# Kernel optimization log

Hardware: AMD Instinct MI355X
Metric: run time of the kernel (lower is better)

## Reference

```python
import jax, jax.numpy as jnp
import numpy as np

D_MODEL = 1024
N_HEADS = 16
EPS = 1e-5


def layernorm(x, w, b):
    mu = jnp.mean(x, axis=-1, keepdims=True)
    var = jnp.mean(jnp.square(x - mu), axis=-1, keepdims=True)
    return (x - mu) * jax.lax.rsqrt(var + EPS) * w + b


def setup_inputs() -> dict:
    key = jax.random.key(0)
    ks = jax.random.split(key, 8)
    n, s, d = 2, 2048, D_MODEL
    x = jax.random.normal(ks[0], (n, s, d), dtype=jnp.float32)
    padding_mask = jax.random.bernoulli(ks[1], 0.9, (n, s))
    # Linear weights stored as [in, out] (transpose of torch layout; same math)
    qkv_w = jax.random.normal(ks[2], (d, 3 * d), dtype=jnp.float32) / np.sqrt(d)
    qkv_b = jnp.zeros((3 * d,), dtype=jnp.float32)
    out_w = jax.random.normal(ks[3], (d, d), dtype=jnp.float32) / np.sqrt(d)
    out_b = jnp.zeros((d,), dtype=jnp.float32)
    ln_in_w = jnp.ones((d,), dtype=jnp.float32)
    ln_in_b = jnp.zeros((d,), dtype=jnp.float32)
    ln_out_w = jnp.ones((d,), dtype=jnp.float32)
    ln_out_b = jnp.zeros((d,), dtype=jnp.float32)
    return {"x": x, "padding_mask": padding_mask,
            "ln_in_w": ln_in_w, "ln_in_b": ln_in_b,
            "qkv_w": qkv_w, "qkv_b": qkv_b,
            "out_w": out_w, "out_b": out_b,
            "ln_out_w": ln_out_w, "ln_out_b": ln_out_b}


def reference(x, padding_mask, ln_in_w, ln_in_b, qkv_w, qkv_b, out_w, out_b, ln_out_w, ln_out_b):
    n, s, d = x.shape
    h = N_HEADS
    hd = d // h
    xn = layernorm(x, ln_in_w, ln_in_b)
    qkv = (xn @ qkv_w + qkv_b).reshape(n, s, 3, h, hd)  # [n,s,3,h,hd]
    q, k, v = qkv[:, :, 0], qkv[:, :, 1], qkv[:, :, 2]
    # [n,h,t,T]
    attn_logits = jnp.einsum('nthd,nThd->nhtT', q, k) / np.sqrt(hd).astype(np.float32)
    attn_logits = jnp.where(padding_mask[:, None, None, :], attn_logits, jnp.float32(-1e30))
    attn_weights = jax.nn.softmax(attn_logits, axis=-1)
    attn = jnp.einsum('nhtT,nThd->nthd', attn_weights, v)  # [n,t,h,hd]
    attn_vec = attn.reshape(n, s, d)
    return layernorm(attn_vec @ out_w + out_b, ln_out_w, ln_out_b)
```

## Files before the change

kernel.cpp:

```cpp
#include <hip/hip_runtime.h>
#include <math.h>

#define D_MODEL 1024
#define SEQ     2048
#define NBATCH  2
#define NTOK    (NBATCH * SEQ)
#define NH      16
#define HD      64

typedef float f32x4 __attribute__((ext_vector_type(4)));
typedef short bf16x8 __attribute__((ext_vector_type(8)));
typedef short bf16x4 __attribute__((ext_vector_type(4)));

__device__ __forceinline__ unsigned short f2bf(float f) {
  unsigned u = __builtin_bit_cast(unsigned, f);
  u += 0x7FFFu + ((u >> 16) & 1u);
  return (unsigned short)(u >> 16);
}

__device__ __forceinline__ unsigned cvt_pk_bf16(float lo, float hi) {
  unsigned d;
  asm("v_cvt_pk_bf16_f32 %0, %1, %2" : "=v"(d) : "v"(lo), "v"(hi));
  return d;
}

__device__ __forceinline__ f32x4 mfma16(bf16x4 a, bf16x4 b, f32x4 c) {
  return __builtin_amdgcn_mfma_f32_16x16x16bf16_1k(a, b, c, 0, 0, 0);
}

__device__ __forceinline__ void gload16(const void* g, void* l) {
  __builtin_amdgcn_global_load_lds(
      (const __attribute__((address_space(1))) void*)g,
      (__attribute__((address_space(3))) void*)l, 16, 0, 0);
}

__global__ void mask_detect_kernel(const unsigned char* __restrict__ m,
                                   int* __restrict__ flag) {
  __shared__ int c1s, c3s;
  if (threadIdx.x == 0) { c1s = 0; c3s = 0; }
  __syncthreads();
  int c1 = 0, c3 = 0;
  for (int i = threadIdx.x; i < NTOK; i += 256) {
    unsigned char v = m[i];
    if (v) {
      if ((i & 3) == 1) c1++;
      if ((i & 3) == 3) c3++;
    }
  }
  if (c1) atomicAdd(&c1s, c1);
  if (c3) atomicAdd(&c3s, c3);
  __syncthreads();
  if (threadIdx.x == 0) *flag = (c1s > 0) ? 1 : ((c3s > 0) ? 2 : 0);
}

__global__ void mask_convert_kernel(const void* __restrict__ m,
                                    const int* __restrict__ flag,
                                    float* __restrict__ maskMul) {
  int i = blockIdx.x * 256 + threadIdx.x;
  if (i >= NTOK) return;
  int f = *flag;
  bool on;
  if (f == 1)      on = ((const unsigned char*)m)[i] != 0;
  else if (f == 2) on = ((const float*)m)[i] != 0.0f;
  else             on = ((const int*)m)[i] != 0;
  maskMul[i] = on ? 1.0f : 0.0f;
}

__device__ inline float block_reduce_sum(float v, float* red) {
  #pragma unroll
  for (int s = 1; s < 64; s <<= 1) v += __shfl_xor(v, s);
  int wid = threadIdx.x >> 6, lane = threadIdx.x & 63;
  if (lane == 0) red[wid] = v;
  __syncthreads();
  float t = red[0] + red[1] + red[2] + red[3];
  __syncthreads();
  return t;
}

template <bool BF16OUT>
__global__ __launch_bounds__(256) void ln_kernel(const float* __restrict__ x,
                                                 const float* __restrict__ w,
                                                 const float* __restrict__ b,
                                                 void* __restrict__ yv) {
  __shared__ float red[4];
  int row = blockIdx.x;
  int tid = threadIdx.x;
  float4 v = ((const float4*)(x + (size_t)row * D_MODEL))[tid];
  float s = v.x + v.y + v.z + v.w;
  float tot = block_reduce_sum(s, red);
  float mu = tot * (1.0f / D_MODEL);
  float dx = v.x - mu, dy = v.y - mu, dz = v.z - mu, dw = v.w - mu;
  float sq = dx * dx + dy * dy + dz * dz + dw * dw;
  float tot2 = block_reduce_sum(sq, red);
  float inv = rsqrtf(tot2 * (1.0f / D_MODEL) + 1e-5f);
  float4 wv = ((const float4*)w)[tid];
  float4 bv = ((const float4*)b)[tid];
  float4 o;
  o.x = dx * inv * wv.x + bv.x;
  o.y = dy * inv * wv.y + bv.y;
  o.z = dz * inv * wv.z + bv.z;
  o.w = dw * inv * wv.w + bv.w;
  if constexpr (BF16OUT) {
    ushort4 o4 = {f2bf(o.x), f2bf(o.y), f2bf(o.z), f2bf(o.w)};
    ((ushort4*)((unsigned short*)yv + (size_t)row * D_MODEL))[tid] = o4;
  } else {
    ((float4*)((float*)yv + (size_t)row * D_MODEL))[tid] = o;
  }
}

__global__ __launch_bounds__(256) void transpose_convert_kernel(
    const float* __restrict__ W, unsigned short* __restrict__ WT, int K, int N) {
  __shared__ float t[64][65];
  int k0 = blockIdx.y * 64, n0 = blockIdx.x * 64;
  int tid = threadIdx.x;
  int rr = tid >> 4, cc = (tid & 15) * 4;
  #pragma unroll
  for (int i = 0; i < 4; i++) {
    int rk = i * 16 + rr;
    float4 v = *(const float4*)&W[(size_t)(k0 + rk) * N + n0 + cc];
    t[rk][cc + 0] = v.x; t[rk][cc + 1] = v.y; t[rk][cc + 2] = v.z; t[rk][cc + 3] = v.w;
  }
  __syncthreads();
  #pragma unroll
  for (int i = 0; i < 4; i++) {
    int rn = i * 16 + rr;
    ushort4 o = {f2bf(t[cc + 0][rn]), f2bf(t[cc + 1][rn]),
                 f2bf(t[cc + 2][rn]), f2bf(t[cc + 3][rn])};
    *(ushort4*)&WT[(size_t)(n0 + rn) * K + k0 + cc] = o;
  }
}

__global__ __launch_bounds__(256) void v_transpose_kernel(
    const unsigned short* __restrict__ qkv, unsigned short* __restrict__ Vt) {
  __shared__ unsigned short t[64][66];
  int s0 = blockIdx.x * 64;
  int h = blockIdx.y, n = blockIdx.z;
  int tid = threadIdx.x;
  #pragma unroll
  for (int i = 0; i < 2; i++) {
    int ch = i * 256 + tid;
    int sr = ch >> 3, c8 = (ch & 7) * 8;
    const unsigned short* src =
        qkv + (size_t)(n * SEQ + s0 + sr) * 3072 + 2048 + h * 64 + c8;
    uint4 v = *(const uint4*)src;
    unsigned short tmp[8];
    *(uint4*)tmp = v;
    #pragma unroll
    for (int j = 0; j < 8; j++) t[sr][c8 + j] = tmp[j];
  }
  __syncthreads();
  #pragma unroll
  for (int i = 0; i < 2; i++) {
    int ch = i * 256 + tid;
    int d = ch >> 3, s8 = (ch & 7) * 8;
    unsigned short tmp[8];
    #pragma unroll
    for (int j = 0; j < 8; j++) tmp[j] = t[s8 + j][d];
    unsigned short* dst =
        Vt + ((size_t)((n * NH + h) * HD) + d) * SEQ + s0 + s8;
    *(uint4*)dst = *(const uint4*)tmp;
  }
}

template <typename OutT>
__global__ __launch_bounds__(256) void gemm_mfma_kernel(
    const unsigned short* __restrict__ A, const unsigned short* __restrict__ BT,
    const float* __restrict__ bias, OutT* __restrict__ C, int M, int N, int K) {
  __shared__ __align__(16) char As[16384];
  __shared__ __align__(16) char Bs[16384];
  int tid = threadIdx.x;
  int lane = tid & 63, w = tid >> 6;
  int r = lane & 15, g = lane >> 4;
  int wm = w >> 1, wn = w & 1;
  int m0 = blockIdx.y * 128, n0 = blockIdx.x * 128;
  f32x4 acc[4][4] = {};

  const char* Ab = (const char*)A;
  const char* Bb = (const char*)BT;
  for (int k0 = 0; k0 < K; k0 += 64) {
    __syncthreads();
    #pragma unroll
    for (int i = 0; i < 4; i++) {
      int chb = i * 256 + w * 64;
      int ch = chb + lane;
      int row = ch >> 3, cb = (ch & 7) ^ (row & 7);
      gload16(Ab + (((size_t)(m0 + row) * K + k0) << 1) + (cb << 4), As + chb * 16);
      gload16(Bb + (((size_t)(n0 + row) * K + k0) << 1) + (cb << 4), Bs + chb * 16);
    }
    __syncthreads();
    #pragma unroll
    for (int s = 0; s < 2; s++) {
      bf16x8 af[4], bfr[4];
      #pragma unroll
      for (int mt = 0; mt < 4; mt++) {
        int arow = wm * 64 + mt * 16 + r;
        int cb = (s * 4 + g) ^ (arow & 7);
        af[mt] = *(const bf16x8*)(As + arow * 128 + cb * 16);
      }
      #pragma unroll
      for (int nt = 0; nt < 4; nt++) {
        int brow = wn * 64 + nt * 16 + r;
        int cb = (s * 4 + g) ^ (brow & 7);
        bfr[nt] = *(const bf16x8*)(Bs + brow * 128 + cb * 16);
      }
      #pragma unroll
      for (int mt = 0; mt < 4; mt++)
        #pragma unroll
        for (int nt = 0; nt < 4; nt++)
          acc[mt][nt] = __builtin_amdgcn_mfma_f32_16x16x32_bf16(
              af[mt], bfr[nt], acc[mt][nt], 0, 0, 0);
    }
  }
  #pragma unroll
  for (int nt = 0; nt < 4; nt++) {
    int col = n0 + wn * 64 + nt * 16 + r;
    float bv = bias[col];
    #pragma unroll
    for (int mt = 0; mt < 4; mt++) {
      #pragma unroll
      for (int rr = 0; rr < 4; rr++) {
        int row = m0 + wm * 64 + mt * 16 + g * 4 + rr;
        float v = acc[mt][nt][rr] + bv;
        if constexpr (sizeof(OutT) == 2) {
          C[(size_t)row * N + col] = (OutT)f2bf(v);
        } else {
          C[(size_t)row * N + col] = v;
        }
      }
    }
  }
}

__global__ __launch_bounds__(512, 4) void attn_mfma_kernel(
    const unsigned short* __restrict__ qkv, const unsigned short* __restrict__ Vt,
    const float* __restrict__ maskMulG, unsigned short* __restrict__ av) {
  __shared__ __align__(16) char Q_s[16384];
  __shared__ __align__(16) char K_s[2][8192];
  __shared__ __align__(16) char V_s[2][8192];
  int tid = threadIdx.x;
  int lane = tid & 63, w = tid >> 6;
  int r = lane & 15, g = lane >> 4;
  int qt = blockIdx.x, h = blockIdx.y, bn = blockIdx.z;
  size_t tok0 = (size_t)bn * SEQ;

  const char* qb = (const char*)qkv + (((tok0 + qt * 128) * 3072) + h * 64) * 2;
  const char* kb0 = (const char*)qkv + ((tok0 * 3072) + 1024 + h * 64) * 2;
  const char* vb0 = (const char*)Vt + (((size_t)(bn * NH + h) * HD) * SEQ) * 2;

  #pragma unroll
  for (int i = 0; i < 2; i++) {
    int chb = i * 512 + w * 64;
    int ch = chb + lane;
    int row = ch >> 3, cb = (ch & 7) ^ (row & 7);
    gload16(qb + (size_t)row * 6144 + (cb << 4), Q_s + chb * 16);
  }
  auto stage_kv = [&](int kt, int buf) {
    int chb = w * 64;
    int ch = chb + lane;
    int row = ch >> 3, cb = (ch & 7) ^ (row & 7);
    gload16(kb0 + (size_t)(kt * 64 + row) * 6144 + (cb << 4), K_s[buf] + chb * 16);
    gload16(vb0 + (size_t)row * 4096 + (size_t)kt * 128 + (cb << 4), V_s[buf] + chb * 16);
  };
  stage_kv(0, 0);
  __syncthreads();

  float mstate = -30000.0f;
  float lstate = 0.f;
  f32x4 o_acc[4] = {};

  const float CC = 0.18033688011112042f;
  const float DEFER = 44.3614195558365f;

  for (int kt = 0; kt < SEQ / 64; kt++) {
    int cur = kt & 1;
    float4 mmv[4];
    #pragma unroll
    for (int nt = 0; nt < 4; nt++)
      mmv[nt] = *(const float4*)(maskMulG + tok0 + kt * 64 + nt * 16 + 4 * g);
    if (kt + 1 < SEQ / 64) stage_kv(kt + 1, cur ^ 1);

    f32x4 sa[4] = {};
    #pragma unroll
    for (int s = 0; s < 2; s++) {
      int qrow = w * 16 + r;
      int cbq = (s * 4 + g) ^ (qrow & 7);
      bf16x8 qf = *(const bf16x8*)(Q_s + qrow * 128 + cbq * 16);
      #pragma unroll
      for (int nt = 0; nt < 4; nt++) {
        int krow = nt * 16 + r;
        int cb = (s * 4 + g) ^ (krow & 7);
        bf16x8 kf = *(const bf16x8*)(K_s[cur] + krow * 128 + cb * 16);
        sa[nt] = __builtin_amdgcn_mfma_f32_16x16x32_bf16(kf, qf, sa[nt], 0, 0, 0);
      }
    }

    float sv[16];
    #pragma unroll
    for (int nt = 0; nt < 4; nt++)
      #pragma unroll
      for (int rr = 0; rr < 4; rr++) sv[nt * 4 + rr] = sa[nt][rr];
    float m01 = fmaxf(sv[0], sv[1]),   m23 = fmaxf(sv[2], sv[3]);
    float m45 = fmaxf(sv[4], sv[5]),   m67 = fmaxf(sv[6], sv[7]);
    float m89 = fmaxf(sv[8], sv[9]),   mab = fmaxf(sv[10], sv[11]);
    float mcd = fmaxf(sv[12], sv[13]), mef = fmaxf(sv[14], sv[15]);
    float mx = fmaxf(fmaxf(fmaxf(m01, m23), fmaxf(m45, m67)),
                     fmaxf(fmaxf(m89, mab), fmaxf(mcd, mef)));
    mx = fmaxf(mx, __shfl_xor(mx, 16));
    mx = fmaxf(mx, __shfl_xor(mx, 32));
    if (__any(mx > mstate + DEFER)) {
      float mnew = fmaxf(mstate, mx);
      float alpha = exp2f((mstate - mnew) * CC);
      lstate *= alpha;
      #pragma unroll
      for (int dt = 0; dt < 4; dt++) o_acc[dt] *= alpha;
      mstate = mnew;
    }
    float mc = mstate * CC;
    float p[16];
    float rs = 0.f;
    #pragma unroll
    for (int nt = 0; nt < 4; nt++) {
      float q0 = exp2f(fmaf(sv[nt * 4 + 0], CC, -mc)) * ((const float*)&mmv[nt])[0];
      float q1 = exp2f(fmaf(sv[nt * 4 + 1], CC, -mc)) * ((const float*)&mmv[nt])[1];
      float q2 = exp2f(fmaf(sv[nt * 4 + 2], CC, -mc)) * ((const float*)&mmv[nt])[2];
      float q3 = exp2f(fmaf(sv[nt * 4 + 3], CC, -mc)) * ((const float*)&mmv[nt])[3];
      p[nt * 4 + 0] = q0; p[nt * 4 + 1] = q1; p[nt * 4 + 2] = q2; p[nt * 4 + 3] = q3;
      rs += (q0 + q1) + (q2 + q3);
    }
    rs += __shfl_xor(rs, 16);
    rs += __shfl_xor(rs, 32);
    lstate += rs;

    bf16x4 bq[4];
    #pragma unroll
    for (int s4 = 0; s4 < 4; s4++) {
      uint2 u;
      u.x = cvt_pk_bf16(p[4 * s4 + 0], p[4 * s4 + 1]);
      u.y = cvt_pk_bf16(p[4 * s4 + 2], p[4 * s4 + 3]);
      bq[s4] = __builtin_bit_cast(bf16x4, u);
    }
    #pragma unroll
    for (int s4 = 0; s4 < 4; s4++) {
      #pragma unroll
      for (int dt = 0; dt < 4; dt++) {
        int row = dt * 16 + r;
        int chunk = (2 * s4 + (g >> 1)) ^ (row & 7);
        bf16x4 vf = *(const bf16x4*)(V_s[cur] + row * 128 + chunk * 16 + (g & 1) * 8);
        o_acc[dt] = mfma16(vf, bq[s4], o_acc[dt]);
      }
    }
    __syncthreads();
  }

  float invl = 1.0f / fmaxf(lstate, 1e-30f);
  size_t qrow = tok0 + (size_t)qt * 128 + w * 16 + r;
  unsigned short* base = av + qrow * D_MODEL + h * 64;
  #pragma unroll
  for (int dt = 0; dt < 4; dt++) {
    ushort4 o4 = {f2bf(o_acc[dt][0] * invl), f2bf(o_acc[dt][1] * invl),
                  f2bf(o_acc[dt][2] * invl), f2bf(o_acc[dt][3] * invl)};
    *(ushort4*)(base + dt * 16 + 4 * g) = o4;
  }
}

extern "C" void kernel_launch(void* const* d_in, const int* in_sizes, int n_in,
                              void* d_out, int out_size, void* d_ws, size_t ws_size,
                              hipStream_t stream) {
  const float* x        = (const float*)d_in[0];
  const void*  mask     = d_in[1];
  const float* ln_in_w  = (const float*)d_in[2];
  const float* ln_in_b  = (const float*)d_in[3];
  const float* qkv_w    = (const float*)d_in[4];
  const float* qkv_b    = (const float*)d_in[5];
  const float* out_w    = (const float*)d_in[6];
  const float* out_b    = (const float*)d_in[7];
  const float* ln_out_w = (const float*)d_in[8];
  const float* ln_out_b = (const float*)d_in[9];
  float* out = (float*)d_out;

  const size_t MB = 1024 * 1024;
  char* ws = (char*)d_ws;
  unsigned short* xn      = (unsigned short*)(ws);
  unsigned short* qkv     = (unsigned short*)(ws + 8 * MB);
  unsigned short* Vt      = (unsigned short*)(ws + 32 * MB);
  unsigned short* av      = (unsigned short*)(ws + 40 * MB);
  float*          proj    = (float*)(ws + 48 * MB);
  unsigned short* qkv_wT  = (unsigned short*)(ws + 64 * MB);
  unsigned short* out_wT  = (unsigned short*)(ws + 70 * MB);
  float*          maskMul = (float*)(ws + 72 * MB);
  int*            flag    = (int*)(ws + 72 * MB + 16384);

  mask_detect_kernel<<<1, 256, 0, stream>>>((const unsigned char*)mask, flag);
  mask_convert_kernel<<<(NTOK + 255) / 256, 256, 0, stream>>>(mask, flag, maskMul);

  transpose_convert_kernel<<<dim3(3 * D_MODEL / 64, D_MODEL / 64), 256, 0, stream>>>(
      qkv_w, qkv_wT, D_MODEL, 3 * D_MODEL);
  transpose_convert_kernel<<<dim3(D_MODEL / 64, D_MODEL / 64), 256, 0, stream>>>(
      out_w, out_wT, D_MODEL, D_MODEL);

  ln_kernel<true><<<NTOK, 256, 0, stream>>>(x, ln_in_w, ln_in_b, xn);

  gemm_mfma_kernel<unsigned short><<<dim3(3 * D_MODEL / 128, NTOK / 128), 256, 0, stream>>>(
      xn, qkv_wT, qkv_b, qkv, NTOK, 3 * D_MODEL, D_MODEL);

  v_transpose_kernel<<<dim3(SEQ / 64, NH, NBATCH), 256, 0, stream>>>(qkv, Vt);

  attn_mfma_kernel<<<dim3(SEQ / 128, NH, NBATCH), 512, 0, stream>>>(
      qkv, Vt, maskMul, av);

  gemm_mfma_kernel<float><<<dim3(D_MODEL / 128, NTOK / 128), 256, 0, stream>>>(
      av, out_wT, out_b, proj, NTOK, D_MODEL, D_MODEL);

  ln_kernel<false><<<NTOK, 256, 0, stream>>>(proj, ln_out_w, ln_out_b, out);
}
```

Before: 178.6 us.

## Merge mask and weight-prep kernels, store projection output as bf16

Folds mask type detection into the convert kernel, so every block recomputes the flag from a scan of the whole mask. The two weight transpose launches become one combined launch. The output projection GEMM now writes bf16 instead of fp32, and the final layernorm reads bf16. This removes two kernel launches and halves the projection's write and read traffic, at the cost of extra rounding before the final layernorm and redundant per-block mask scans.

Result: faster. 173.0 us (-3.1%).

```diff
diff --git a/kernel.cpp b/kernel.cpp
--- a/kernel.cpp
+++ b/kernel.cpp
@@ -18,6 +18,10 @@
   return (unsigned short)(u >> 16);
 }
 
+__device__ __forceinline__ float bf2f(unsigned short h) {
+  return __builtin_bit_cast(float, (unsigned)h << 16);
+}
+
 __device__ __forceinline__ unsigned cvt_pk_bf16(float lo, float hi) {
   unsigned d;
   asm("v_cvt_pk_bf16_f32 %0, %1, %2" : "=v"(d) : "v"(lo), "v"(hi));
@@ -34,14 +38,15 @@
       (__attribute__((address_space(3))) void*)l, 16, 0, 0);
 }
 
-__global__ void mask_detect_kernel(const unsigned char* __restrict__ m,
-                                   int* __restrict__ flag) {
+__global__ __launch_bounds__(256) void mask_convert_kernel(
+    const void* __restrict__ m, float* __restrict__ maskMul) {
   __shared__ int c1s, c3s;
   if (threadIdx.x == 0) { c1s = 0; c3s = 0; }
   __syncthreads();
+  const unsigned char* mb = (const unsigned char*)m;
   int c1 = 0, c3 = 0;
   for (int i = threadIdx.x; i < NTOK; i += 256) {
-    unsigned char v = m[i];
+    unsigned char v = mb[i];
     if (v) {
       if ((i & 3) == 1) c1++;
       if ((i & 3) == 3) c3++;
@@ -50,17 +55,11 @@
   if (c1) atomicAdd(&c1s, c1);
   if (c3) atomicAdd(&c3s, c3);
   __syncthreads();
-  if (threadIdx.x == 0) *flag = (c1s > 0) ? 1 : ((c3s > 0) ? 2 : 0);
-}
-
-__global__ void mask_convert_kernel(const void* __restrict__ m,
-                                    const int* __restrict__ flag,
-                                    float* __restrict__ maskMul) {
+  int f = (c1s > 0) ? 1 : ((c3s > 0) ? 2 : 0);
   int i = blockIdx.x * 256 + threadIdx.x;
   if (i >= NTOK) return;
-  int f = *flag;
   bool on;
-  if (f == 1)      on = ((const unsigned char*)m)[i] != 0;
+  if (f == 1)      on = mb[i] != 0;
   else if (f == 2) on = ((const float*)m)[i] != 0.0f;
   else             on = ((const int*)m)[i] != 0;
   maskMul[i] = on ? 1.0f : 0.0f;
@@ -77,15 +76,21 @@
   return t;
 }
 
-template <bool BF16OUT>
-__global__ __launch_bounds__(256) void ln_kernel(const float* __restrict__ x,
+template <bool BF16IN, bool BF16OUT>
+__global__ __launch_bounds__(256) void ln_kernel(const void* __restrict__ xv,
                                                  const float* __restrict__ w,
                                                  const float* __restrict__ b,
                                                  void* __restrict__ yv) {
   __shared__ float red[4];
   int row = blockIdx.x;
   int tid = threadIdx.x;
-  float4 v = ((const float4*)(x + (size_t)row * D_MODEL))[tid];
+  float4 v;
+  if constexpr (BF16IN) {
+    ushort4 u = ((const ushort4*)((const unsigned short*)xv + (size_t)row * D_MODEL))[tid];
+    v.x = bf2f(u.x); v.y = bf2f(u.y); v.z = bf2f(u.z); v.w = bf2f(u.w);
+  } else {
+    v = ((const float4*)((const float*)xv + (size_t)row * D_MODEL))[tid];
+  }
   float s = v.x + v.y + v.z + v.w;
   float tot = block_reduce_sum(s, red);
   float mu = tot * (1.0f / D_MODEL);
@@ -108,10 +113,18 @@
   }
 }
 
-__global__ __launch_bounds__(256) void transpose_convert_kernel(
-    const float* __restrict__ W, unsigned short* __restrict__ WT, int K, int N) {
+__global__ __launch_bounds__(256) void transpose_convert2_kernel(
+    const float* __restrict__ Wq, unsigned short* __restrict__ WTq,
+    const float* __restrict__ Wo, unsigned short* __restrict__ WTo) {
   __shared__ float t[64][65];
-  int k0 = blockIdx.y * 64, n0 = blockIdx.x * 64;
+  int bx = blockIdx.x;
+  const float* W;
+  unsigned short* WT;
+  int N, n0;
+  if (bx < 48) { W = Wq; WT = WTq; N = 3072; n0 = bx * 64; }
+  else         { W = Wo; WT = WTo; N = 1024; n0 = (bx - 48) * 64; }
+  const int K = 1024;
+  int k0 = blockIdx.y * 64;
   int tid = threadIdx.x;
   int rr = tid >> 4, cc = (tid & 15) * 4;
   #pragma unroll
@@ -384,21 +397,17 @@
   unsigned short* qkv     = (unsigned short*)(ws + 8 * MB);
   unsigned short* Vt      = (unsigned short*)(ws + 32 * MB);
   unsigned short* av      = (unsigned short*)(ws + 40 * MB);
-  float*          proj    = (float*)(ws + 48 * MB);
+  unsigned short* proj    = (unsigned short*)(ws + 48 * MB);
   unsigned short* qkv_wT  = (unsigned short*)(ws + 64 * MB);
   unsigned short* out_wT  = (unsigned short*)(ws + 70 * MB);
   float*          maskMul = (float*)(ws + 72 * MB);
-  int*            flag    = (int*)(ws + 72 * MB + 16384);
-
-  mask_detect_kernel<<<1, 256, 0, stream>>>((const unsigned char*)mask, flag);
-  mask_convert_kernel<<<(NTOK + 255) / 256, 256, 0, stream>>>(mask, flag, maskMul);
-
-  transpose_convert_kernel<<<dim3(3 * D_MODEL / 64, D_MODEL / 64), 256, 0, stream>>>(
-      qkv_w, qkv_wT, D_MODEL, 3 * D_MODEL);
-  transpose_convert_kernel<<<dim3(D_MODEL / 64, D_MODEL / 64), 256, 0, stream>>>(
-      out_w, out_wT, D_MODEL, D_MODEL);
-
-  ln_kernel<true><<<NTOK, 256, 0, stream>>>(x, ln_in_w, ln_in_b, xn);
+
+  mask_convert_kernel<<<(NTOK + 255) / 256, 256, 0, stream>>>(mask, maskMul);
+
+  transpose_convert2_kernel<<<dim3(64, 16), 256, 0, stream>>>(
+      qkv_w, qkv_wT, out_w, out_wT);
+
+  ln_kernel<false, true><<<NTOK, 256, 0, stream>>>(x, ln_in_w, ln_in_b, xn);
 
   gemm_mfma_kernel<unsigned short><<<dim3(3 * D_MODEL / 128, NTOK / 128), 256, 0, stream>>>(
       xn, qkv_wT, qkv_b, qkv, NTOK, 3 * D_MODEL, D_MODEL);
@@ -408,8 +417,8 @@
   attn_mfma_kernel<<<dim3(SEQ / 128, NH, NBATCH), 512, 0, stream>>>(
       qkv, Vt, maskMul, av);
 
-  gemm_mfma_kernel<float><<<dim3(D_MODEL / 128, NTOK / 128), 256, 0, stream>>>(
+  gemm_mfma_kernel<unsigned short><<<dim3(D_MODEL / 128, NTOK / 128), 256, 0, stream>>>(
       av, out_wT, out_b, proj, NTOK, D_MODEL, D_MODEL);
 
-  ln_kernel<false><<<NTOK, 256, 0, stream>>>(proj, ln_out_w, ln_out_b, out);
-}
+  ln_kernel<true, false><<<NTOK, 256, 0, stream>>>(proj, ln_out_w, ln_out_b, out);
+}
```
